# Kernel tuning notes

Hardware: AMD Instinct MI355X
Metric: run time of the kernel (lower is better)

The kernel has to match this reference:

```python
import jax, jax.numpy as jnp
import numpy as np

PATCH = 96
STRIDE = PATCH // 2  # 48


def setup_inputs() -> dict:
    key = jax.random.key(0)
    kx = jax.random.fold_in(key, 0)
    x = jax.random.uniform(kx, (8, 4, 1056, 1056), dtype=jnp.float32)
    mu_pristine = jnp.zeros((36,), dtype=jnp.float32)
    cov_pristine = jnp.eye(36, dtype=jnp.float32)
    return {"x": x, "mu_pristine": mu_pristine, "cov_pristine": cov_pristine}


def _extract_patches(x):
    # x: [B, C, H, W] -> overlapping patches [B, C, N, P, P], stride = P//2
    B, C, H, W = x.shape
    nH = (H - PATCH) // STRIDE + 1
    nW = (W - PATCH) // STRIDE + 1
    idx_h = np.arange(nH)[:, None] * STRIDE + np.arange(PATCH)[None, :]  # [nH, P]
    idx_w = np.arange(nW)[:, None] * STRIDE + np.arange(PATCH)[None, :]  # [nW, P]
    p = x[:, :, idx_h, :]            # [B, C, nH, P, W]
    p = p[:, :, :, :, idx_w]         # [B, C, nH, P, nW, P]
    p = p.transpose(0, 1, 2, 4, 3, 5)  # [B, C, nH, nW, P, P]
    return p.reshape(B, C, nH * nW, PATCH, PATCH)


def reference(x, mu_pristine, cov_pristine):
    patches = _extract_patches(x)  # [B, C, N, P, P]
    mu = patches.mean(axis=(-2, -1))                    # [B, C, N]
    var = patches.var(axis=(-2, -1), ddof=1)            # unbiased, matches torch.var
    gx = jnp.diff(patches, axis=-1)                     # [B, C, N, P, P-1]
    gy = jnp.diff(patches, axis=-2)                     # [B, C, N, P-1, P]
    grad_mag = jnp.sqrt((gx * gx).mean(axis=(-2, -1)) + (gy * gy).mean(axis=(-2, -1)))
    # torch concatenates [mu, var, grad_mag] along channel dim per patch, then means over patches
    feats = jnp.concatenate([mu, var, grad_mag], axis=1).mean(axis=-1)  # [B, 3C]
    d = feats.shape[1]
    mu0 = mu_pristine[:d]
    cov_inv = jnp.linalg.inv(cov_pristine[:d, :d])
    diff = feats - mu0[None, :]
    dist = jnp.sqrt(((diff @ cov_inv) * diff).sum(axis=1))  # Mahalanobis distance [B]
    return dist.mean()
```

## Files before the change

### kernel.cpp

```cpp
#include <hip/hip_runtime.h>
#include <math.h>

#define PATCH 96
#define STRIDE 48
#define NH 21
#define NW 21
#define NP (NH * NW)
#define BATCH 8
#define CHAN 4
#define NBC (BATCH * CHAN)
#define IMG_H 1056
#define IMG_W 1056
#define NBAND 22
#define NCHUNK 22
#define NSTAT 6
#define NPIX 9216.0f
#define NGRAD 9120.0f

__global__ __launch_bounds__(320) void band_stats_kernel(
    const float* __restrict__ x, float* __restrict__ pf) {
  __shared__ float acc[NCHUNK * NSTAT];

  const int t = threadIdx.x;
  const int bc = blockIdx.x / NBAND;
  const int band = blockIdx.x - bc * NBAND;
  const bool active = t < 264;
  const int tc = active ? t : 263;
  const int lane = t & 63;

  const float* rowbase = x + (size_t)bc * (IMG_H * IMG_W)
                           + (size_t)(band * STRIDE) * IMG_W
                           + (size_t)(4 * tc);
  const int rmax = (band == NBAND - 1) ? 47 : 48;

  float s1 = 0.f, s2 = 0.f, gxi = 0.f, gxb = 0.f, gyi = 0.f, gyb = 0.f;
  float4 prev = make_float4(0.f, 0.f, 0.f, 0.f);
  const bool bnd_is_gxb = ((t % 12) == 11);

  for (int r = 0; r <= rmax; ++r) {
    const float4 A = *(const float4*)(rowbase + (size_t)r * IMG_W);
    if (r < 48) {
      s1 += A.x + A.y + A.z + A.w;
      s2 += A.x * A.x + A.y * A.y + A.z * A.z + A.w * A.w;
      float nxt = __shfl_down(A.x, 1);
      if (lane == 63 && t < 263) nxt = rowbase[(size_t)r * IMG_W + 4];
      float d1 = A.y - A.x, d2 = A.z - A.y, d3 = A.w - A.z, d4 = nxt - A.w;
      gxi += d1 * d1 + d2 * d2 + d3 * d3;
      float bd = d4 * d4;
      if (bnd_is_gxb) gxb += bd; else gxi += bd;
    }
    if (r > 0) {
      float e0 = A.x - prev.x, e1 = A.y - prev.y,
            e2 = A.z - prev.z, e3 = A.w - prev.w;
      float g = e0 * e0 + e1 * e1 + e2 * e2 + e3 * e3;
      if (r < 48) gyi += g; else gyb += g;
    }
    prev = A;
  }

  for (int i = t; i < NCHUNK * NSTAT; i += 320) acc[i] = 0.f;
  __syncthreads();
  if (active) {
    const int chunk = t / 12;
    atomicAdd(&acc[chunk * NSTAT + 0], s1);
    atomicAdd(&acc[chunk * NSTAT + 1], s2);
    atomicAdd(&acc[chunk * NSTAT + 2], gxi);
    atomicAdd(&acc[chunk * NSTAT + 3], gxb);
    atomicAdd(&acc[chunk * NSTAT + 4], gyi);
    atomicAdd(&acc[chunk * NSTAT + 5], gyb);
  }
  __syncthreads();
  float* dst = pf + (size_t)(bc * NBAND + band) * (NCHUNK * NSTAT);
  for (int i = t; i < NCHUNK * NSTAT; i += 320) dst[i] = acc[i];
}

__global__ __launch_bounds__(512) void patch_feats_kernel(
    const float* __restrict__ pf, float* __restrict__ featsG) {
  __shared__ float S[NBAND * NCHUNK * NSTAT];
  __shared__ float wsum[8][3];

  const int bc = blockIdx.x;
  const int t = threadIdx.x;
  const float* src = pf + (size_t)bc * (NBAND * NCHUNK * NSTAT);
  for (int i = t; i < NBAND * NCHUNK * NSTAT; i += 512) S[i] = src[i];
  __syncthreads();

  float fmu = 0.f, fvar = 0.f, fg = 0.f;
  if (t < NP) {
    const int ph = t / NW, pw = t - ph * NW;
#define AT(b, c, s) S[((b) * NCHUNK + (c)) * NSTAT + (s)]
    float S1 = AT(ph, pw, 0) + AT(ph, pw + 1, 0) + AT(ph + 1, pw, 0) + AT(ph + 1, pw + 1, 0);
    float S2 = AT(ph, pw, 1) + AT(ph, pw + 1, 1) + AT(ph + 1, pw, 1) + AT(ph + 1, pw + 1, 1);
    float Gx = AT(ph, pw, 2) + AT(ph, pw, 3) + AT(ph, pw + 1, 2)
             + AT(ph + 1, pw, 2) + AT(ph + 1, pw, 3) + AT(ph + 1, pw + 1, 2);
    float Gy = AT(ph, pw, 4) + AT(ph, pw, 5) + AT(ph + 1, pw, 4)
             + AT(ph, pw + 1, 4) + AT(ph, pw + 1, 5) + AT(ph + 1, pw + 1, 4);
#undef AT
    fmu = S1 / NPIX;
    fvar = (S2 - S1 * S1 / NPIX) / (NPIX - 1.f);
    fg = sqrtf((Gx + Gy) / NGRAD);
  }
#pragma unroll
  for (int off = 32; off > 0; off >>= 1) {
    fmu += __shfl_xor(fmu, off);
    fvar += __shfl_xor(fvar, off);
    fg += __shfl_xor(fg, off);
  }
  const int wave = t >> 6;
  if ((t & 63) == 0) { wsum[wave][0] = fmu; wsum[wave][1] = fvar; wsum[wave][2] = fg; }
  __syncthreads();
  if (t == 0) {
    float m = 0.f, v = 0.f, g = 0.f;
#pragma unroll
    for (int w = 0; w < 8; ++w) { m += wsum[w][0]; v += wsum[w][1]; g += wsum[w][2]; }
    const int b = bc / CHAN, c = bc - b * CHAN;
    featsG[b * 12 + 0 + c] = m / (float)NP;
    featsG[b * 12 + 4 + c] = v / (float)NP;
    featsG[b * 12 + 8 + c] = g / (float)NP;
  }
}

__global__ __launch_bounds__(320) void finalize_kernel(
    const float* __restrict__ featsG, const float* __restrict__ mu0_full,
    const float* __restrict__ cov_full, float* __restrict__ out) {
  __shared__ double M[12][24];
  __shared__ float feats_s[96];
  __shared__ float dist[BATCH];
  __shared__ int pr_s;

  const int t = threadIdx.x;
  if (t < 96) feats_s[t] = featsG[t];
  if (t < 288) {
    const int r = t / 24, c = t - r * 24;
    M[r][c] = (c < 12) ? (double)cov_full[r * 36 + c] : ((c - 12 == r) ? 1.0 : 0.0);
  }
  __syncthreads();

  for (int k = 0; k < 12; ++k) {
    if (t == 0) {
      int pr = k; double best = fabs(M[k][k]);
      for (int r = k + 1; r < 12; ++r) {
        double a = fabs(M[r][k]);
        if (a > best) { best = a; pr = r; }
      }
      pr_s = pr;
    }
    __syncthreads();
    const int pr = pr_s;
    if (pr != k && t < 24) { double tmp = M[k][t]; M[k][t] = M[pr][t]; M[pr][t] = tmp; }
    __syncthreads();
    const double piv = M[k][k];
    __syncthreads();
    if (t < 24) M[k][t] = M[k][t] / piv;
    __syncthreads();
    double f = 0.0, mkc = 0.0;
    const int r = t / 24, c = t - r * 24;
    if (t < 288) { f = M[r][k]; mkc = M[k][c]; }
    __syncthreads();
    if (t < 288 && r != k) M[r][c] -= f * mkc;
    __syncthreads();
  }

  if (t < BATCH) {
    double acc = 0.0;
    for (int i = 0; i < 12; ++i) {
      double di = (double)feats_s[t * 12 + i] - (double)mu0_full[i];
      for (int j = 0; j < 12; ++j) {
        double dj = (double)feats_s[t * 12 + j] - (double)mu0_full[j];
        acc += di * M[i][12 + j] * dj;
      }
    }
    dist[t] = (float)sqrt(acc);
  }
  __syncthreads();
  if (t == 0) {
    float m = 0.f;
#pragma unroll
    for (int b = 0; b < BATCH; ++b) m += dist[b];
    out[0] = m / (float)BATCH;
  }
}

extern "C" void kernel_launch(void* const* d_in, const int* in_sizes, int n_in,
                              void* d_out, int out_size, void* d_ws, size_t ws_size,
                              hipStream_t stream) {
  const float* x   = (const float*)d_in[0];
  const float* mu0 = (const float*)d_in[1];
  const float* cov = (const float*)d_in[2];
  float* out = (float*)d_out;
  float* pf     = (float*)d_ws;
  float* featsG = pf + (size_t)NBC * NBAND * NCHUNK * NSTAT;

  band_stats_kernel<<<NBC * NBAND, 320, 0, stream>>>(x, pf);
  patch_feats_kernel<<<NBC, 512, 0, stream>>>(pf, featsG);
  finalize_kernel<<<1, 320, 0, stream>>>(featsG, mu0, cov, out);
}
```

Baseline: 239.5 us.

## Split band rows across two thread teams and invert covariance in registers

The band statistics kernel now uses 576 threads arranged as two teams, each covering 24 of the 48 band rows. This halves the serial row loop per thread and doubles the memory-level parallelism per block. The horizontal neighbour is now read directly from global memory instead of being passed by a wave shuffle, and the loop is partially unrolled. The finalize kernel replaces the shared-memory Gauss-Jordan elimination, which needed many barriers, with a single wave that uses register shuffles, and it drops partial pivoting, which trades numerical robustness for fewer barriers.

```diff
diff --git a/kernel.cpp b/kernel.cpp
--- a/kernel.cpp
+++ b/kernel.cpp
@@ -17,51 +17,68 @@
 #define NPIX 9216.0f
 #define NGRAD 9120.0f
 
-__global__ __launch_bounds__(320) void band_stats_kernel(
+__global__ __launch_bounds__(576) void band_stats_kernel(
     const float* __restrict__ x, float* __restrict__ pf) {
   __shared__ float acc[NCHUNK * NSTAT];
 
   const int t = threadIdx.x;
   const int bc = blockIdx.x / NBAND;
   const int band = blockIdx.x - bc * NBAND;
-  const bool active = t < 264;
-  const int tc = active ? t : 263;
-  const int lane = t & 63;
+  const int team = (t >= 288) ? 1 : 0;
+  const int tt = t - 288 * team;
+  const bool active = tt < 264;
+  const int tc = active ? tt : 263;
+  const int noff = (tc == 263) ? 3 : 4;
+  const int r0 = team * 24;
 
   const float* rowbase = x + (size_t)bc * (IMG_H * IMG_W)
-                           + (size_t)(band * STRIDE) * IMG_W
+                           + (size_t)(band * STRIDE + r0) * IMG_W
                            + (size_t)(4 * tc);
-  const int rmax = (band == NBAND - 1) ? 47 : 48;
 
   float s1 = 0.f, s2 = 0.f, gxi = 0.f, gxb = 0.f, gyi = 0.f, gyb = 0.f;
-  float4 prev = make_float4(0.f, 0.f, 0.f, 0.f);
-  const bool bnd_is_gxb = ((t % 12) == 11);
-
-  for (int r = 0; r <= rmax; ++r) {
+  const bool bnd_is_gxb = ((tc % 12) == 11);
+
+#define SUMS_GX(A, nxt)                                                  \
+  do {                                                                   \
+    s1 += (A).x + (A).y + (A).z + (A).w;                                 \
+    s2 += (A).x * (A).x + (A).y * (A).y + (A).z * (A).z + (A).w * (A).w; \
+    float d1 = (A).y - (A).x, d2 = (A).z - (A).y, d3 = (A).w - (A).z;    \
+    float d4 = (nxt) - (A).w;                                            \
+    gxi += d1 * d1 + d2 * d2 + d3 * d3;                                  \
+    float bd = d4 * d4;                                                  \
+    if (bnd_is_gxb) gxb += bd; else gxi += bd;                           \
+  } while (0)
+
+  float4 prev;
+  {
+    const float4 A = *(const float4*)rowbase;
+    const float nxt = rowbase[noff];
+    SUMS_GX(A, nxt);
+    prev = A;
+  }
+#pragma unroll 4
+  for (int r = 1; r < 24; ++r) {
     const float4 A = *(const float4*)(rowbase + (size_t)r * IMG_W);
-    if (r < 48) {
-      s1 += A.x + A.y + A.z + A.w;
-      s2 += A.x * A.x + A.y * A.y + A.z * A.z + A.w * A.w;
-      float nxt = __shfl_down(A.x, 1);
-      if (lane == 63 && t < 263) nxt = rowbase[(size_t)r * IMG_W + 4];
-      float d1 = A.y - A.x, d2 = A.z - A.y, d3 = A.w - A.z, d4 = nxt - A.w;
-      gxi += d1 * d1 + d2 * d2 + d3 * d3;
-      float bd = d4 * d4;
-      if (bnd_is_gxb) gxb += bd; else gxi += bd;
-    }
-    if (r > 0) {
-      float e0 = A.x - prev.x, e1 = A.y - prev.y,
-            e2 = A.z - prev.z, e3 = A.w - prev.w;
-      float g = e0 * e0 + e1 * e1 + e2 * e2 + e3 * e3;
-      if (r < 48) gyi += g; else gyb += g;
-    }
+    const float nxt = rowbase[(size_t)r * IMG_W + noff];
+    SUMS_GX(A, nxt);
+    const float e0 = A.x - prev.x, e1 = A.y - prev.y,
+                e2 = A.z - prev.z, e3 = A.w - prev.w;
+    gyi += e0 * e0 + e1 * e1 + e2 * e2 + e3 * e3;
     prev = A;
   }
-
-  for (int i = t; i < NCHUNK * NSTAT; i += 320) acc[i] = 0.f;
+  if (team == 0 || band != NBAND - 1) {
+    const float4 A = *(const float4*)(rowbase + (size_t)24 * IMG_W);
+    const float e0 = A.x - prev.x, e1 = A.y - prev.y,
+                e2 = A.z - prev.z, e3 = A.w - prev.w;
+    const float g = e0 * e0 + e1 * e1 + e2 * e2 + e3 * e3;
+    if (team == 0) gyi += g; else gyb += g;
+  }
+#undef SUMS_GX
+
+  for (int i = t; i < NCHUNK * NSTAT; i += 576) acc[i] = 0.f;
   __syncthreads();
   if (active) {
-    const int chunk = t / 12;
+    const int chunk = tc / 12;
     atomicAdd(&acc[chunk * NSTAT + 0], s1);
     atomicAdd(&acc[chunk * NSTAT + 1], s2);
     atomicAdd(&acc[chunk * NSTAT + 2], gxi);
@@ -71,7 +88,7 @@
   }
   __syncthreads();
   float* dst = pf + (size_t)(bc * NBAND + band) * (NCHUNK * NSTAT);
-  for (int i = t; i < NCHUNK * NSTAT; i += 320) dst[i] = acc[i];
+  for (int i = t; i < NCHUNK * NSTAT; i += 576) dst[i] = acc[i];
 }
 
 __global__ __launch_bounds__(512) void patch_feats_kernel(
@@ -120,55 +137,58 @@
   }
 }
 
-__global__ __launch_bounds__(320) void finalize_kernel(
+__global__ __launch_bounds__(64) void finalize_kernel(
     const float* __restrict__ featsG, const float* __restrict__ mu0_full,
     const float* __restrict__ cov_full, float* __restrict__ out) {
-  __shared__ double M[12][24];
   __shared__ float feats_s[96];
+  __shared__ double inv_s[12][12];
   __shared__ float dist[BATCH];
-  __shared__ int pr_s;
 
   const int t = threadIdx.x;
-  if (t < 96) feats_s[t] = featsG[t];
-  if (t < 288) {
-    const int r = t / 24, c = t - r * 24;
-    M[r][c] = (c < 12) ? (double)cov_full[r * 36 + c] : ((c - 12 == r) ? 1.0 : 0.0);
-  }
-  __syncthreads();
-
+  feats_s[t] = featsG[t];
+  if (t < 32) feats_s[64 + t] = featsG[64 + t];
+
+  double M[12];
+#pragma unroll
+  for (int r = 0; r < 12; ++r) {
+    double v = 0.0;
+    if (t < 12) v = (double)cov_full[r * 36 + t];
+    else if (t < 24) v = (t - 12 == r) ? 1.0 : 0.0;
+    M[r] = v;
+  }
+
+#pragma unroll
   for (int k = 0; k < 12; ++k) {
-    if (t == 0) {
-      int pr = k; double best = fabs(M[k][k]);
-      for (int r = k + 1; r < 12; ++r) {
-        double a = fabs(M[r][k]);
-        if (a > best) { best = a; pr = r; }
-      }
-      pr_s = pr;
+    const double piv = __shfl(M[k], k);
+    const double ip = 1.0 / piv;
+    M[k] *= ip;
+#pragma unroll
+    for (int r = 0; r < 12; ++r) {
+      if (r == k) continue;
+      const double f = __shfl(M[r], k);
+      M[r] -= f * M[k];
     }
-    __syncthreads();
-    const int pr = pr_s;
-    if (pr != k && t < 24) { double tmp = M[k][t]; M[k][t] = M[pr][t]; M[pr][t] = tmp; }
-    __syncthreads();
-    const double piv = M[k][k];
-    __syncthreads();
-    if (t < 24) M[k][t] = M[k][t] / piv;
-    __syncthreads();
-    double f = 0.0, mkc = 0.0;
-    const int r = t / 24, c = t - r * 24;
-    if (t < 288) { f = M[r][k]; mkc = M[k][c]; }
-    __syncthreads();
-    if (t < 288 && r != k) M[r][c] -= f * mkc;
-    __syncthreads();
-  }
+  }
+
+  if (t >= 12 && t < 24) {
+    const int j = t - 12;
+#pragma unroll
+    for (int r = 0; r < 12; ++r) inv_s[r][j] = M[r];
+  }
+  __syncthreads();
 
   if (t < BATCH) {
     double acc = 0.0;
+    double d[12];
+#pragma unroll
+    for (int i = 0; i < 12; ++i)
+      d[i] = (double)feats_s[t * 12 + i] - (double)mu0_full[i];
+#pragma unroll
     for (int i = 0; i < 12; ++i) {
-      double di = (double)feats_s[t * 12 + i] - (double)mu0_full[i];
-      for (int j = 0; j < 12; ++j) {
-        double dj = (double)feats_s[t * 12 + j] - (double)mu0_full[j];
-        acc += di * M[i][12 + j] * dj;
-      }
+      double row = 0.0;
+#pragma unroll
+      for (int j = 0; j < 12; ++j) row += inv_s[i][j] * d[j];
+      acc += d[i] * row;
     }
     dist[t] = (float)sqrt(acc);
   }
@@ -191,7 +211,7 @@
   float* pf     = (float*)d_ws;
   float* featsG = pf + (size_t)NBC * NBAND * NCHUNK * NSTAT;
 
-  band_stats_kernel<<<NBC * NBAND, 320, 0, stream>>>(x, pf);
+  band_stats_kernel<<<NBC * NBAND, 576, 0, stream>>>(x, pf);
   patch_feats_kernel<<<NBC, 512, 0, stream>>>(pf, featsG);
-  finalize_kernel<<<1, 320, 0, stream>>>(featsG, mu0, cov, out);
-}
+  finalize_kernel<<<1, 64, 0, stream>>>(featsG, mu0, cov, out);
+}
```

After: 228.4 us. 4.6% less time.
